# Kernel optimization log

Measured on AMD Instinct MI355X. Metric: run time of the kernel, lower is better.

The kernel has to match this reference:

```python
import jax, jax.numpy as jnp
import numpy as np

LAYER_START = 4
WIN = 2          # context_window_size (over the LAYER axis)
NORM_EPS = 1e-12 # F.normalize eps
COS_EPS = 1e-8   # cosine_similarity eps


def _alpha_for_k(sf, k, nlay):
    """Alignment/novelty weights for layer k. sf: [B, Ttok, Lay, H].
    Mirrors torch: left = tf[k-w:k] (empty when k<w due to python slicing),
    right = tf[k+1:k+w+1], self row last; QR of window_matrix.T."""
    left = list(range(k - WIN, k)) if k >= WIN else []
    right = list(range(k + 1, min(k + WIN + 1, nlay)))
    rows = left + right + [k]
    m = len(rows)  # 3..5
    W = sf[:, :, jnp.array(rows), :]          # [B,T,m,H]
    A = jnp.swapaxes(W, -1, -2)               # [B,T,H,m]  (window_matrix.T)
    _, R = jnp.linalg.qr(A)                   # reduced: R [B,T,m,m]
    r = R[..., :, -1]                         # [B,T,m]
    Rsub = R[..., :-1, :-1]                   # [B,T,m-1,m-1]
    coln = Rsub / jnp.maximum(jnp.linalg.norm(Rsub, axis=-2, keepdims=True), NORM_EPS)
    row_mean = jnp.mean(coln, axis=-1)        # mean over columns -> [B,T,m-1]
    align = jnp.sum(row_mean * R[..., :-1, -1], axis=-1) / jnp.linalg.norm(r[..., :-1], axis=-1)
    align = 1.0 / (align * m * 2)
    novelty = jnp.abs(r[..., -1]) / jnp.linalg.norm(r, axis=-1)
    return align, novelty


def wk_forward(all_hidden_states, attention_mask):
    # [NL,B,T,H] -> [B, Lay, T, H] after layer_start slice
    emb = jnp.transpose(all_hidden_states, (1, 0, 2, 3))[:, LAYER_START:, :, :]
    B, Lay, T, H = emb.shape
    ntok = T - 1  # attention_mask is all-ones: unmask_num = sum(mask) - 1
    sf = jnp.transpose(emb[:, :, :ntok, :], (0, 2, 1, 3))  # [B,Ttok,Lay,H]
    aligns, novs = [], []
    for k in range(Lay):  # small fixed loop over 9 layers
        a, n = _alpha_for_k(sf, k, Lay)
        aligns.append(a)
        novs.append(n)
    align = jnp.stack(aligns, axis=-1)  # [B,Ttok,Lay]
    nov = jnp.stack(novs, axis=-1)
    align = align / jnp.sum(align, axis=-1, keepdims=True)
    nov = nov / jnp.sum(nov, axis=-1, keepdims=True)
    alpha = align + nov
    alpha = alpha / jnp.sum(alpha, axis=-1, keepdims=True)
    token_emb = jnp.einsum('btl,btlh->bth', alpha, sf)  # unify_token output per token
    # unify_sentence: per-token variance (unbiased) of consecutive-layer cosine sims
    a, b = sf[:, :, 1:, :], sf[:, :, :-1, :]
    num = jnp.sum(a * b, axis=-1)
    den = jnp.maximum(jnp.linalg.norm(a, axis=-1) * jnp.linalg.norm(b, axis=-1), COS_EPS)
    sims = num / den                              # [B,Ttok,Lay-1]
    var_tok = jnp.var(sims, axis=-1, ddof=1)      # torch.var default unbiased
    var_tok = var_tok / jnp.sum(var_tok, axis=-1, keepdims=True)
    return jnp.einsum('bt,bth->bh', var_tok, token_emb)  # [B,H]


def setup_inputs() -> dict:
    key = jax.random.key(0)
    NL, B, T, H = 13, 8, 512, 768
    all_hidden_states = jax.random.normal(key, (NL, B, T, H), dtype=jnp.float32)
    attention_mask = jnp.ones((B, T), dtype=jnp.int32)
    return {"all_hidden_states": all_hidden_states, "attention_mask": attention_mask}


def reference(all_hidden_states, attention_mask):
    return wk_forward(all_hidden_states, attention_mask)
```

## Files before the change

### kernel.cpp

```cpp
#include <hip/hip_runtime.h>
#include <math.h>

#define B_DIM 8
#define T_DIM 512
#define H_DIM 768
#define NTOK 511
#define NLAY 9
#define LAYER_START 4
#define NBAND 35
#define TCHUNK 128

__device__ float g_part[B_DIM * TCHUNK * H_DIM];
__device__ float g_varp[B_DIM * TCHUNK];

#define BOFF(d) ((d)*9 - (d) * ((d)-1) / 2)

template <int CTRL>
__device__ __forceinline__ float dpp_mov(float x) {
  return __builtin_bit_cast(
      float, __builtin_amdgcn_update_dpp(0, __builtin_bit_cast(int, x), CTRL,
                                         0xF, 0xF, true));
}

__device__ __forceinline__ float wave_sum_dpp(float x) {
  x += dpp_mov<0x111>(x);
  x += dpp_mov<0x112>(x);
  x += dpp_mov<0x114>(x);
  x += dpp_mov<0x118>(x);
  x += dpp_mov<0x142>(x);
  x += dpp_mov<0x143>(x);
  return x;
}

__global__ __launch_bounds__(256, 2) void wk_a(const float* __restrict__ ahs) {
  const int chunk = blockIdx.x;
  const int b = blockIdx.y;
  const int wave = threadIdx.x >> 6;
  const int lane = threadIdx.x & 63;
  const int t_raw = chunk * 4 + wave;
  const bool active = (t_raw < NTOK);
  const int t = active ? t_raw : (NTOK - 1);

  __shared__ float sG[4][36];
  __shared__ float lds_out[4][H_DIM];
  __shared__ float lds_var[4];

  const size_t LSTR = (size_t)B_DIM * T_DIM * H_DIM;
  const float* lay0 =
      ahs + (size_t)LAYER_START * LSTR + ((size_t)b * T_DIM + t) * H_DIM;

  float4 v[NLAY][3];
#pragma unroll
  for (int l = 0; l < NLAY; ++l) {
    const float* base = lay0 + (size_t)l * LSTR;
#pragma unroll
    for (int s = 0; s < 3; ++s) {
      v[l][s] = *reinterpret_cast<const float4*>(base + s * 256 + lane * 4);
    }
  }

  float g[NBAND];
#pragma unroll
  for (int d = 0; d <= 4; ++d) {
#pragma unroll
    for (int i = 0; i + d < NLAY; ++i) {
      float s0 = 0.f;
#pragma unroll
      for (int s = 0; s < 3; ++s) {
        const float4 x = v[i][s], y = v[i + d][s];
        s0 += x.x * y.x + x.y * y.y + x.z * y.z + x.w * y.w;
      }
      g[BOFF(d) + i] = s0;
    }
  }

#pragma unroll
  for (int p = 0; p < NBAND; ++p) g[p] = wave_sum_dpp(g[p]);

  if (lane == 63) {
#pragma unroll
    for (int p = 0; p < NBAND; ++p) sG[wave][p] = g[p];
  }
  __syncthreads();

  const int k = lane < NLAY ? lane : NLAY - 1;
  const int nl = (k >= 2) ? 2 : 0;
  const int nrr = (NLAY - 1 - k) < 2 ? (NLAY - 1 - k) : 2;
  const int m = nl + nrr + 1;

  auto rowf = [&](int i) -> int {
    return (i < nl) ? (k - 2 + i) : ((i < nl + nrr) ? (k + 1 + i - nl) : k);
  };
  auto GK = [&](int i, int j) -> float {
    int a = rowf(i), c = rowf(j);
    int lo = a < c ? a : c;
    int d = (a < c ? c : a) - lo;
    return sG[wave][d * 9 - d * (d - 1) / 2 + lo];
  };

  float R[5][5];
#pragma unroll
  for (int j = 0; j < 5; ++j)
#pragma unroll
    for (int i = 0; i < 5; ++i) R[i][j] = 0.f;

#pragma unroll
  for (int j = 0; j < 5; ++j) {
    if (j < m) {
#pragma unroll
      for (int i = 0; i < 5; ++i) {
        if (i < j) {
          float s = GK(i, j);
#pragma unroll
          for (int p = 0; p < 4; ++p)
            if (p < i) s -= R[p][i] * R[p][j];
          R[i][j] = s / R[i][i];
        }
      }
      float sjj = GK(j, j);
#pragma unroll
      for (int p = 0; p < 4; ++p)
        if (p < j) sjj -= R[p][j] * R[p][j];
      R[j][j] = sqrtf(fmaxf(sjj, 0.f));
    }
  }

  float r[5];
#pragma unroll
  for (int i = 0; i < 5; ++i)
    r[i] = (m == 3) ? R[i][2] : ((m == 4) ? R[i][3] : R[i][4]);

  float rowmean[4] = {0.f, 0.f, 0.f, 0.f};
#pragma unroll
  for (int j = 0; j < 4; ++j) {
    if (j < m - 1) {
      float cn = 0.f;
#pragma unroll
      for (int i = 0; i < 4; ++i)
        if (i <= j) cn += R[i][j] * R[i][j];
      cn = fmaxf(sqrtf(cn), 1e-12f);
      float inv = 1.f / cn;
#pragma unroll
      for (int i = 0; i < 4; ++i)
        if (i < m - 1) rowmean[i] += R[i][j] * inv;
    }
  }

  const float inv_m1 = 1.f / (float)(m - 1);
  float dotv = 0.f, nrm2 = 0.f;
#pragma unroll
  for (int i = 0; i < 4; ++i) {
    if (i < m - 1) {
      dotv += (rowmean[i] * inv_m1) * r[i];
      nrm2 += r[i] * r[i];
    }
  }
  float align_raw = dotv / sqrtf(nrm2);
  float align_v = 1.f / (align_raw * (float)m * 2.f);
  float rlast = (m == 3) ? r[2] : ((m == 4) ? r[3] : r[4]);
  float nov_v = fabsf(rlast) / sqrtf(nrm2 + rlast * rlast);

  float al[NLAY], nv[NLAY];
  float asum = 0.f, nsum = 0.f;
#pragma unroll
  for (int l = 0; l < NLAY; ++l) {
    al[l] = __shfl(align_v, l, 64);
    nv[l] = __shfl(nov_v, l, 64);
    asum += al[l];
    nsum += nv[l];
  }
  float alpha[NLAY];
  float csum = 0.f;
#pragma unroll
  for (int l = 0; l < NLAY; ++l) {
    alpha[l] = al[l] / asum + nv[l] / nsum;
    csum += alpha[l];
  }
  const float inv_csum = 1.f / csum;

  float sims[NLAY - 1];
  float smean = 0.f;
#pragma unroll
  for (int j = 0; j < NLAY - 1; ++j) {
    float num = sG[wave][BOFF(1) + j];
    float den = fmaxf(sqrtf(sG[wave][j]) * sqrtf(sG[wave][j + 1]), 1e-8f);
    sims[j] = num / den;
    smean += sims[j];
  }
  smean *= (1.f / 8.f);
  float var = 0.f;
#pragma unroll
  for (int j = 0; j < NLAY - 1; ++j) {
    float d = sims[j] - smean;
    var += d * d;
  }
  var *= (1.f / 7.f);
  if (!active) var = 0.f;

  if (lane == 0) lds_var[wave] = var;

  float c[NLAY];
#pragma unroll
  for (int l = 0; l < NLAY; ++l) c[l] = var * alpha[l] * inv_csum;

#pragma unroll
  for (int s = 0; s < 3; ++s) {
    float4 o;
    o.x = 0.f; o.y = 0.f; o.z = 0.f; o.w = 0.f;
#pragma unroll
    for (int l = 0; l < NLAY; ++l) {
      o.x += c[l] * v[l][s].x;
      o.y += c[l] * v[l][s].y;
      o.z += c[l] * v[l][s].z;
      o.w += c[l] * v[l][s].w;
    }
    *reinterpret_cast<float4*>(&lds_out[wave][s * 256 + lane * 4]) = o;
  }
  __syncthreads();

  float* dst = g_part + ((size_t)(b * TCHUNK + chunk)) * H_DIM;
#pragma unroll
  for (int s = 0; s < 3; ++s) {
    int h = s * 256 + threadIdx.x;
    float sum = lds_out[0][h] + lds_out[1][h] + lds_out[2][h] + lds_out[3][h];
    dst[h] = sum;
  }
  if (threadIdx.x == 0) {
    g_varp[b * TCHUNK + chunk] =
        lds_var[0] + lds_var[1] + lds_var[2] + lds_var[3];
  }
}

__global__ __launch_bounds__(256) void wk_r(float* __restrict__ out) {
  const int b = blockIdx.y;
  const int h = blockIdx.x * 256 + threadIdx.x;

  float acc = 0.f;
#pragma unroll 8
  for (int j = 0; j < TCHUNK; ++j)
    acc += g_part[((size_t)(b * TCHUNK + j)) * H_DIM + h];

  float ssum = 0.f;
#pragma unroll 8
  for (int j = 0; j < TCHUNK; ++j) ssum += g_varp[b * TCHUNK + j];

  out[b * H_DIM + h] = acc / ssum;
}

extern "C" void kernel_launch(void* const* d_in, const int* in_sizes, int n_in,
                              void* d_out, int out_size, void* d_ws, size_t ws_size,
                              hipStream_t stream) {
  const float* ahs = (const float*)d_in[0];
  float* out = (float*)d_out;
  (void)d_ws; (void)ws_size;

  wk_a<<<dim3(TCHUNK, B_DIM), dim3(256), 0, stream>>>(ahs);
  wk_r<<<dim3(3, B_DIM), dim3(256), 0, stream>>>(out);
}
```

Before: 227.2 us.

## Split fused kernel into gram, per-token tail, weighted-sum and finalize kernels

The single fused kernel, which held all 9 layers in registers, is split into four kernels. A gram kernel streams the layers in 3 slices with lower register pressure. A per-token tail kernel runs the Cholesky/alpha math with one thread per token. A weighted-sum kernel then re-reads the hidden states to accumulate the alpha-weighted sums, followed by a final reduction. This is meant to raise occupancy and remove the lane-serialized QR math from the bandwidth-bound pass, but it reads the input tensor twice and adds launches and global round-trips.

Result: slower. 258.5 us (+13.8%).

```diff
diff --git a/kernel.cpp b/kernel.cpp
--- a/kernel.cpp
+++ b/kernel.cpp
@@ -8,12 +8,14 @@
 #define NLAY 9
 #define LAYER_START 4
 #define NBAND 35
-#define TCHUNK 128
-
-__device__ float g_part[B_DIM * TCHUNK * H_DIM];
-__device__ float g_varp[B_DIM * TCHUNK];
+#define NCHUNK 64
 
 #define BOFF(d) ((d)*9 - (d) * ((d)-1) / 2)
+
+__device__ float g_gram[B_DIM * T_DIM * NBAND];
+__device__ float g_w[B_DIM * NTOK * NLAY];
+__device__ float g_var[B_DIM * NTOK];
+__device__ float g_part[B_DIM * NCHUNK * H_DIM];
 
 template <int CTRL>
 __device__ __forceinline__ float dpp_mov(float x) {
@@ -21,7 +23,6 @@
       float, __builtin_amdgcn_update_dpp(0, __builtin_bit_cast(int, x), CTRL,
                                          0xF, 0xF, true));
 }
-
 __device__ __forceinline__ float wave_sum_dpp(float x) {
   x += dpp_mov<0x111>(x);
   x += dpp_mov<0x112>(x);
@@ -32,45 +33,38 @@
   return x;
 }
 
-__global__ __launch_bounds__(256, 2) void wk_a(const float* __restrict__ ahs) {
+__global__ __launch_bounds__(256, 4) void gram_k(const float* __restrict__ ahs) {
   const int chunk = blockIdx.x;
   const int b = blockIdx.y;
   const int wave = threadIdx.x >> 6;
   const int lane = threadIdx.x & 63;
   const int t_raw = chunk * 4 + wave;
-  const bool active = (t_raw < NTOK);
-  const int t = active ? t_raw : (NTOK - 1);
-
-  __shared__ float sG[4][36];
-  __shared__ float lds_out[4][H_DIM];
-  __shared__ float lds_var[4];
+  const int t = (t_raw < NTOK) ? t_raw : (NTOK - 1);
+
+  __shared__ float sGall[4][NBAND];
 
   const size_t LSTR = (size_t)B_DIM * T_DIM * H_DIM;
   const float* lay0 =
       ahs + (size_t)LAYER_START * LSTR + ((size_t)b * T_DIM + t) * H_DIM;
 
-  float4 v[NLAY][3];
-#pragma unroll
-  for (int l = 0; l < NLAY; ++l) {
-    const float* base = lay0 + (size_t)l * LSTR;
-#pragma unroll
-    for (int s = 0; s < 3; ++s) {
-      v[l][s] = *reinterpret_cast<const float4*>(base + s * 256 + lane * 4);
-    }
-  }
-
   float g[NBAND];
 #pragma unroll
-  for (int d = 0; d <= 4; ++d) {
-#pragma unroll
-    for (int i = 0; i + d < NLAY; ++i) {
-      float s0 = 0.f;
-#pragma unroll
-      for (int s = 0; s < 3; ++s) {
-        const float4 x = v[i][s], y = v[i + d][s];
-        s0 += x.x * y.x + x.y * y.y + x.z * y.z + x.w * y.w;
+  for (int p = 0; p < NBAND; ++p) g[p] = 0.f;
+
+#pragma unroll 1
+  for (int s = 0; s < 3; ++s) {
+    const float* p0 = lay0 + s * 256 + lane * 4;
+    float4 vs[NLAY];
+#pragma unroll
+    for (int l = 0; l < NLAY; ++l)
+      vs[l] = *reinterpret_cast<const float4*>(p0 + (size_t)l * LSTR);
+#pragma unroll
+    for (int d = 0; d <= 4; ++d) {
+#pragma unroll
+      for (int i = 0; i + d < NLAY; ++i) {
+        const float4 x = vs[i], y = vs[i + d];
+        g[BOFF(d) + i] += x.x * y.x + x.y * y.y + x.z * y.z + x.w * y.w;
       }
-      g[BOFF(d) + i] = s0;
     }
   }
 
@@ -79,23 +73,36 @@
 
   if (lane == 63) {
 #pragma unroll
-    for (int p = 0; p < NBAND; ++p) sG[wave][p] = g[p];
+    for (int p = 0; p < NBAND; ++p) sGall[wave][p] = g[p];
   }
   __syncthreads();
 
-  const int k = lane < NLAY ? lane : NLAY - 1;
-  const int nl = (k >= 2) ? 2 : 0;
-  const int nrr = (NLAY - 1 - k) < 2 ? (NLAY - 1 - k) : 2;
-  const int m = nl + nrr + 1;
-
-  auto rowf = [&](int i) -> int {
-    return (i < nl) ? (k - 2 + i) : ((i < nl + nrr) ? (k + 1 + i - nl) : k);
+  const int i = threadIdx.x;
+  if (i < 4 * NBAND) {
+    const int w = i / NBAND;
+    const int p = i - w * NBAND;
+    const int tr = chunk * 4 + w;
+    g_gram[((size_t)(b * T_DIM + tr)) * NBAND + p] = sGall[w][p];
+  }
+}
+
+template <int K>
+__device__ __forceinline__ void chol_one(const float* __restrict__ row,
+                                         float& A_out, float& N_out) {
+  constexpr int nl = (K >= 2) ? 2 : 0;
+  constexpr int nr = ((NLAY - 1 - K) < 2) ? (NLAY - 1 - K) : 2;
+  constexpr int m = nl + nr + 1;
+
+  struct Map {
+    static constexpr int rowf(int i) {
+      return (i < nl) ? (K - 2 + i) : ((i < nl + nr) ? (K + 1 + i - nl) : K);
+    }
   };
   auto GK = [&](int i, int j) -> float {
-    int a = rowf(i), c = rowf(j);
-    int lo = a < c ? a : c;
-    int d = (a < c ? c : a) - lo;
-    return sG[wave][d * 9 - d * (d - 1) / 2 + lo];
+    const int a = Map::rowf(i), c = Map::rowf(j);
+    const int lo = a < c ? a : c;
+    const int d = (a < c ? c : a) - lo;
+    return row[d * 9 - d * (d - 1) / 2 + lo];
   };
 
   float R[5][5];
@@ -127,8 +134,7 @@
 
   float r[5];
 #pragma unroll
-  for (int i = 0; i < 5; ++i)
-    r[i] = (m == 3) ? R[i][2] : ((m == 4) ? R[i][3] : R[i][4]);
+  for (int i = 0; i < 5; ++i) r[i] = R[i][m - 1];
 
   float rowmean[4] = {0.f, 0.f, 0.f, 0.f};
 #pragma unroll
@@ -139,14 +145,14 @@
       for (int i = 0; i < 4; ++i)
         if (i <= j) cn += R[i][j] * R[i][j];
       cn = fmaxf(sqrtf(cn), 1e-12f);
-      float inv = 1.f / cn;
+      const float inv = 1.f / cn;
 #pragma unroll
       for (int i = 0; i < 4; ++i)
         if (i < m - 1) rowmean[i] += R[i][j] * inv;
     }
   }
 
-  const float inv_m1 = 1.f / (float)(m - 1);
+  constexpr float inv_m1 = 1.f / (float)(m - 1);
   float dotv = 0.f, nrm2 = 0.f;
 #pragma unroll
   for (int i = 0; i < 4; ++i) {
@@ -155,20 +161,41 @@
       nrm2 += r[i] * r[i];
     }
   }
-  float align_raw = dotv / sqrtf(nrm2);
-  float align_v = 1.f / (align_raw * (float)m * 2.f);
-  float rlast = (m == 3) ? r[2] : ((m == 4) ? r[3] : r[4]);
-  float nov_v = fabsf(rlast) / sqrtf(nrm2 + rlast * rlast);
+  const float align_raw = dotv / sqrtf(nrm2);
+  A_out = 1.f / (align_raw * (float)m * 2.f);
+  const float rlast = r[m - 1];
+  N_out = fabsf(rlast) / sqrtf(nrm2 + rlast * rlast);
+}
+
+__global__ __launch_bounds__(64) void tail_k() {
+  const int tid = threadIdx.x;
+  const int tok = blockIdx.x * 64 + tid;
+  const bool valid = (tok < B_DIM * NTOK);
+  const int tk = valid ? tok : 0;
+  const int b = tk / NTOK;
+  const int t = tk - b * NTOK;
+
+  __shared__ float sB[64][NBAND + 2];
+
+  const float* gp = g_gram + ((size_t)(b * T_DIM + t)) * NBAND;
+#pragma unroll
+  for (int p = 0; p < NBAND; ++p) sB[tid][p] = gp[p];
+  const float* row = &sB[tid][0];
 
   float al[NLAY], nv[NLAY];
+  chol_one<0>(row, al[0], nv[0]);
+  chol_one<1>(row, al[1], nv[1]);
+  chol_one<2>(row, al[2], nv[2]);
+  chol_one<3>(row, al[3], nv[3]);
+  chol_one<4>(row, al[4], nv[4]);
+  chol_one<5>(row, al[5], nv[5]);
+  chol_one<6>(row, al[6], nv[6]);
+  chol_one<7>(row, al[7], nv[7]);
+  chol_one<8>(row, al[8], nv[8]);
+
   float asum = 0.f, nsum = 0.f;
 #pragma unroll
-  for (int l = 0; l < NLAY; ++l) {
-    al[l] = __shfl(align_v, l, 64);
-    nv[l] = __shfl(nov_v, l, 64);
-    asum += al[l];
-    nsum += nv[l];
-  }
+  for (int l = 0; l < NLAY; ++l) { asum += al[l]; nsum += nv[l]; }
   float alpha[NLAY];
   float csum = 0.f;
 #pragma unroll
@@ -182,8 +209,8 @@
   float smean = 0.f;
 #pragma unroll
   for (int j = 0; j < NLAY - 1; ++j) {
-    float num = sG[wave][BOFF(1) + j];
-    float den = fmaxf(sqrtf(sG[wave][j]) * sqrtf(sG[wave][j + 1]), 1e-8f);
+    const float num = row[BOFF(1) + j];
+    const float den = fmaxf(sqrtf(row[j]) * sqrtf(row[j + 1]), 1e-8f);
     sims[j] = num / den;
     smean += sims[j];
   }
@@ -191,60 +218,63 @@
   float var = 0.f;
 #pragma unroll
   for (int j = 0; j < NLAY - 1; ++j) {
-    float d = sims[j] - smean;
+    const float d = sims[j] - smean;
     var += d * d;
   }
   var *= (1.f / 7.f);
-  if (!active) var = 0.f;
-
-  if (lane == 0) lds_var[wave] = var;
-
-  float c[NLAY];
-#pragma unroll
-  for (int l = 0; l < NLAY; ++l) c[l] = var * alpha[l] * inv_csum;
-
-#pragma unroll
-  for (int s = 0; s < 3; ++s) {
-    float4 o;
-    o.x = 0.f; o.y = 0.f; o.z = 0.f; o.w = 0.f;
+
+  if (valid) {
+#pragma unroll
+    for (int l = 0; l < NLAY; ++l)
+      g_w[(size_t)tok * NLAY + l] = var * alpha[l] * inv_csum;
+    g_var[tok] = var;
+  }
+}
+
+__global__ __launch_bounds__(192) void wsum_k(const float* __restrict__ ahs) {
+  const int c = blockIdx.x;
+  const int b = blockIdx.y;
+  const int h4 = threadIdx.x;
+  const size_t LSTR = (size_t)B_DIM * T_DIM * H_DIM;
+
+  float4 acc;
+  acc.x = 0.f; acc.y = 0.f; acc.z = 0.f; acc.w = 0.f;
+
+#pragma unroll 1
+  for (int tt = 0; tt < 8; ++tt) {
+    const int t = c * 8 + tt;
+    if (t >= NTOK) break;
+    const float* wp = g_w + ((size_t)(b * NTOK + t)) * NLAY;
+    const float* vbase = ahs + (size_t)LAYER_START * LSTR +
+                         ((size_t)b * T_DIM + t) * H_DIM + h4 * 4;
 #pragma unroll
     for (int l = 0; l < NLAY; ++l) {
-      o.x += c[l] * v[l][s].x;
-      o.y += c[l] * v[l][s].y;
-      o.z += c[l] * v[l][s].z;
-      o.w += c[l] * v[l][s].w;
-    }
-    *reinterpret_cast<float4*>(&lds_out[wave][s * 256 + lane * 4]) = o;
-  }
-  __syncthreads();
-
-  float* dst = g_part + ((size_t)(b * TCHUNK + chunk)) * H_DIM;
-#pragma unroll
-  for (int s = 0; s < 3; ++s) {
-    int h = s * 256 + threadIdx.x;
-    float sum = lds_out[0][h] + lds_out[1][h] + lds_out[2][h] + lds_out[3][h];
-    dst[h] = sum;
-  }
-  if (threadIdx.x == 0) {
-    g_varp[b * TCHUNK + chunk] =
-        lds_var[0] + lds_var[1] + lds_var[2] + lds_var[3];
-  }
-}
-
-__global__ __launch_bounds__(256) void wk_r(float* __restrict__ out) {
+      const float wl = wp[l];
+      const float4 vv = *reinterpret_cast<const float4*>(vbase + (size_t)l * LSTR);
+      acc.x += wl * vv.x;
+      acc.y += wl * vv.y;
+      acc.z += wl * vv.z;
+      acc.w += wl * vv.w;
+    }
+  }
+  *reinterpret_cast<float4*>(g_part + ((size_t)(b * NCHUNK + c)) * H_DIM +
+                             h4 * 4) = acc;
+}
+
+__global__ __launch_bounds__(256) void fin_k(float* __restrict__ out) {
   const int b = blockIdx.y;
   const int h = blockIdx.x * 256 + threadIdx.x;
 
   float acc = 0.f;
 #pragma unroll 8
-  for (int j = 0; j < TCHUNK; ++j)
-    acc += g_part[((size_t)(b * TCHUNK + j)) * H_DIM + h];
-
-  float ssum = 0.f;
+  for (int cc = 0; cc < NCHUNK; ++cc)
+    acc += g_part[((size_t)(b * NCHUNK + cc)) * H_DIM + h];
+
+  float sv = 0.f;
 #pragma unroll 8
-  for (int j = 0; j < TCHUNK; ++j) ssum += g_varp[b * TCHUNK + j];
-
-  out[b * H_DIM + h] = acc / ssum;
+  for (int t = 0; t < NTOK; ++t) sv += g_var[b * NTOK + t];
+
+  out[b * H_DIM + h] = acc / sv;
 }
 
 extern "C" void kernel_launch(void* const* d_in, const int* in_sizes, int n_in,
@@ -254,6 +284,8 @@
   float* out = (float*)d_out;
   (void)d_ws; (void)ws_size;
 
-  wk_a<<<dim3(TCHUNK, B_DIM), dim3(256), 0, stream>>>(ahs);
-  wk_r<<<dim3(3, B_DIM), dim3(256), 0, stream>>>(out);
-}
+  gram_k<<<dim3(T_DIM / 4, B_DIM), dim3(256), 0, stream>>>(ahs);
+  tail_k<<<dim3((B_DIM * NTOK + 63) / 64), dim3(64), 0, stream>>>();
+  wsum_k<<<dim3(NCHUNK, B_DIM), dim3(192), 0, stream>>>(ahs);
+  fin_k<<<dim3(3, B_DIM), dim3(256), 0, stream>>>(out);
+}
```

## Split each token across three waves and write per-token partials

Applied to the files above, without the earlier changes.

Work is repartitioned so that one 192-thread block handles one token, with each of its three waves covering a 256-element slice of H. Gram dot products are combined across the waves through shared memory, and a single wave then runs the small QR/alpha math. This cuts per-thread register use (9 float4 loads instead of 27), raising occupancy and memory-level parallelism for the bandwidth-bound load. In exchange, every token writes a full H-length partial to global memory and the final reduction loops over 511 tokens instead of 128 chunks, which adds about 12MB of extra write and read traffic.

Result: slower. 269.8 us (+18.8%).

```diff
diff --git a/kernel.cpp b/kernel.cpp
--- a/kernel.cpp
+++ b/kernel.cpp
@@ -8,12 +8,11 @@
 #define NLAY 9
 #define LAYER_START 4
 #define NBAND 35
-#define TCHUNK 128
-
-__device__ float g_part[B_DIM * TCHUNK * H_DIM];
-__device__ float g_varp[B_DIM * TCHUNK];
 
 #define BOFF(d) ((d)*9 - (d) * ((d)-1) / 2)
+
+__device__ float g_part[B_DIM * NTOK * H_DIM];
+__device__ float g_var[B_DIM * NTOK];
 
 template <int CTRL>
 __device__ __forceinline__ float dpp_mov(float x) {
@@ -21,7 +20,6 @@
       float, __builtin_amdgcn_update_dpp(0, __builtin_bit_cast(int, x), CTRL,
                                          0xF, 0xF, true));
 }
-
 __device__ __forceinline__ float wave_sum_dpp(float x) {
   x += dpp_mov<0x111>(x);
   x += dpp_mov<0x112>(x);
@@ -32,219 +30,199 @@
   return x;
 }
 
-__global__ __launch_bounds__(256, 2) void wk_a(const float* __restrict__ ahs) {
-  const int chunk = blockIdx.x;
+__global__ __launch_bounds__(192, 4) void wk_main(const float* __restrict__ ahs) {
+  const int t = blockIdx.x;
   const int b = blockIdx.y;
-  const int wave = threadIdx.x >> 6;
+  const int w = threadIdx.x >> 6;
   const int lane = threadIdx.x & 63;
-  const int t_raw = chunk * 4 + wave;
-  const bool active = (t_raw < NTOK);
-  const int t = active ? t_raw : (NTOK - 1);
-
-  __shared__ float sG[4][36];
-  __shared__ float lds_out[4][H_DIM];
-  __shared__ float lds_var[4];
+
+  __shared__ float sG[3][NBAND];
+  __shared__ float sGc[NBAND + 1];
+  __shared__ float sC[NLAY + 1];
 
   const size_t LSTR = (size_t)B_DIM * T_DIM * H_DIM;
-  const float* lay0 =
-      ahs + (size_t)LAYER_START * LSTR + ((size_t)b * T_DIM + t) * H_DIM;
-
-  float4 v[NLAY][3];
+  const float* base = ahs + (size_t)LAYER_START * LSTR +
+                      ((size_t)b * T_DIM + t) * H_DIM + w * 256 + lane * 4;
+
+  float4 v[NLAY];
+#pragma unroll
+  for (int l = 0; l < NLAY; ++l)
+    v[l] = *reinterpret_cast<const float4*>(base + (size_t)l * LSTR);
+
+  float g[NBAND];
+#pragma unroll
+  for (int d = 0; d <= 4; ++d) {
+#pragma unroll
+    for (int i = 0; i + d < NLAY; ++i) {
+      const float4 x = v[i], y = v[i + d];
+      g[BOFF(d) + i] = x.x * y.x + x.y * y.y + x.z * y.z + x.w * y.w;
+    }
+  }
+
+#pragma unroll
+  for (int p = 0; p < NBAND; ++p) g[p] = wave_sum_dpp(g[p]);
+
+  if (lane == 63) {
+#pragma unroll
+    for (int p = 0; p < NBAND; ++p) sG[w][p] = g[p];
+  }
+  __syncthreads();
+
+  if (threadIdx.x < NBAND)
+    sGc[threadIdx.x] =
+        sG[0][threadIdx.x] + sG[1][threadIdx.x] + sG[2][threadIdx.x];
+  __syncthreads();
+
+  if (w == 0) {
+    const int k = lane < NLAY ? lane : NLAY - 1;
+    const int nl = (k >= 2) ? 2 : 0;
+    const int nrr = (NLAY - 1 - k) < 2 ? (NLAY - 1 - k) : 2;
+    const int m = nl + nrr + 1;
+
+    auto rowf = [&](int i) -> int {
+      return (i < nl) ? (k - 2 + i) : ((i < nl + nrr) ? (k + 1 + i - nl) : k);
+    };
+    auto GK = [&](int i, int j) -> float {
+      int a = rowf(i), c = rowf(j);
+      int lo = a < c ? a : c;
+      int d = (a < c ? c : a) - lo;
+      return sGc[d * 9 - d * (d - 1) / 2 + lo];
+    };
+
+    float R[5][5];
+#pragma unroll
+    for (int j = 0; j < 5; ++j)
+#pragma unroll
+      for (int i = 0; i < 5; ++i) R[i][j] = 0.f;
+
+#pragma unroll
+    for (int j = 0; j < 5; ++j) {
+      if (j < m) {
+#pragma unroll
+        for (int i = 0; i < 5; ++i) {
+          if (i < j) {
+            float s = GK(i, j);
+#pragma unroll
+            for (int p = 0; p < 4; ++p)
+              if (p < i) s -= R[p][i] * R[p][j];
+            R[i][j] = s / R[i][i];
+          }
+        }
+        float sjj = GK(j, j);
+#pragma unroll
+        for (int p = 0; p < 4; ++p)
+          if (p < j) sjj -= R[p][j] * R[p][j];
+        R[j][j] = sqrtf(fmaxf(sjj, 0.f));
+      }
+    }
+
+    float r[5];
+#pragma unroll
+    for (int i = 0; i < 5; ++i)
+      r[i] = (m == 3) ? R[i][2] : ((m == 4) ? R[i][3] : R[i][4]);
+
+    float rowmean[4] = {0.f, 0.f, 0.f, 0.f};
+#pragma unroll
+    for (int j = 0; j < 4; ++j) {
+      if (j < m - 1) {
+        float cn = 0.f;
+#pragma unroll
+        for (int i = 0; i < 4; ++i)
+          if (i <= j) cn += R[i][j] * R[i][j];
+        cn = fmaxf(sqrtf(cn), 1e-12f);
+        const float inv = 1.f / cn;
+#pragma unroll
+        for (int i = 0; i < 4; ++i)
+          if (i < m - 1) rowmean[i] += R[i][j] * inv;
+      }
+    }
+
+    const float inv_m1 = 1.f / (float)(m - 1);
+    float dotv = 0.f, nrm2 = 0.f;
+#pragma unroll
+    for (int i = 0; i < 4; ++i) {
+      if (i < m - 1) {
+        dotv += (rowmean[i] * inv_m1) * r[i];
+        nrm2 += r[i] * r[i];
+      }
+    }
+    const float align_raw = dotv / sqrtf(nrm2);
+    const float align_v = 1.f / (align_raw * (float)m * 2.f);
+    const float rlast = (m == 3) ? r[2] : ((m == 4) ? r[3] : r[4]);
+    const float nov_v = fabsf(rlast) / sqrtf(nrm2 + rlast * rlast);
+
+    float al[NLAY], nv[NLAY];
+    float asum = 0.f, nsum = 0.f;
+#pragma unroll
+    for (int l = 0; l < NLAY; ++l) {
+      al[l] = __shfl(align_v, l, 64);
+      nv[l] = __shfl(nov_v, l, 64);
+      asum += al[l];
+      nsum += nv[l];
+    }
+    float alpha[NLAY];
+    float csum = 0.f;
+#pragma unroll
+    for (int l = 0; l < NLAY; ++l) {
+      alpha[l] = al[l] / asum + nv[l] / nsum;
+      csum += alpha[l];
+    }
+    const float inv_csum = 1.f / csum;
+
+    float sims[NLAY - 1];
+    float smean = 0.f;
+#pragma unroll
+    for (int j = 0; j < NLAY - 1; ++j) {
+      const float num = sGc[BOFF(1) + j];
+      const float den = fmaxf(sqrtf(sGc[j]) * sqrtf(sGc[j + 1]), 1e-8f);
+      sims[j] = num / den;
+      smean += sims[j];
+    }
+    smean *= (1.f / 8.f);
+    float var = 0.f;
+#pragma unroll
+    for (int j = 0; j < NLAY - 1; ++j) {
+      const float d = sims[j] - smean;
+      var += d * d;
+    }
+    var *= (1.f / 7.f);
+
+    if (lane < NLAY) sC[lane] = var * alpha[lane] * inv_csum;
+    if (lane == 0) g_var[b * NTOK + t] = var;
+  }
+  __syncthreads();
+
+  float c[NLAY];
+#pragma unroll
+  for (int l = 0; l < NLAY; ++l) c[l] = sC[l];
+
+  float4 o;
+  o.x = 0.f; o.y = 0.f; o.z = 0.f; o.w = 0.f;
 #pragma unroll
   for (int l = 0; l < NLAY; ++l) {
-    const float* base = lay0 + (size_t)l * LSTR;
-#pragma unroll
-    for (int s = 0; s < 3; ++s) {
-      v[l][s] = *reinterpret_cast<const float4*>(base + s * 256 + lane * 4);
-    }
-  }
-
-  float g[NBAND];
-#pragma unroll
-  for (int d = 0; d <= 4; ++d) {
-#pragma unroll
-    for (int i = 0; i + d < NLAY; ++i) {
-      float s0 = 0.f;
-#pragma unroll
-      for (int s = 0; s < 3; ++s) {
-        const float4 x = v[i][s], y = v[i + d][s];
-        s0 += x.x * y.x + x.y * y.y + x.z * y.z + x.w * y.w;
-      }
-      g[BOFF(d) + i] = s0;
-    }
-  }
-
-#pragma unroll
-  for (int p = 0; p < NBAND; ++p) g[p] = wave_sum_dpp(g[p]);
-
-  if (lane == 63) {
-#pragma unroll
-    for (int p = 0; p < NBAND; ++p) sG[wave][p] = g[p];
-  }
-  __syncthreads();
-
-  const int k = lane < NLAY ? lane : NLAY - 1;
-  const int nl = (k >= 2) ? 2 : 0;
-  const int nrr = (NLAY - 1 - k) < 2 ? (NLAY - 1 - k) : 2;
-  const int m = nl + nrr + 1;
-
-  auto rowf = [&](int i) -> int {
-    return (i < nl) ? (k - 2 + i) : ((i < nl + nrr) ? (k + 1 + i - nl) : k);
-  };
-  auto GK = [&](int i, int j) -> float {
-    int a = rowf(i), c = rowf(j);
-    int lo = a < c ? a : c;
-    int d = (a < c ? c : a) - lo;
-    return sG[wave][d * 9 - d * (d - 1) / 2 + lo];
-  };
-
-  float R[5][5];
-#pragma unroll
-  for (int j = 0; j < 5; ++j)
-#pragma unroll
-    for (int i = 0; i < 5; ++i) R[i][j] = 0.f;
-
-#pragma unroll
-  for (int j = 0; j < 5; ++j) {
-    if (j < m) {
-#pragma unroll
-      for (int i = 0; i < 5; ++i) {
-        if (i < j) {
-          float s = GK(i, j);
-#pragma unroll
-          for (int p = 0; p < 4; ++p)
-            if (p < i) s -= R[p][i] * R[p][j];
-          R[i][j] = s / R[i][i];
-        }
-      }
-      float sjj = GK(j, j);
-#pragma unroll
-      for (int p = 0; p < 4; ++p)
-        if (p < j) sjj -= R[p][j] * R[p][j];
-      R[j][j] = sqrtf(fmaxf(sjj, 0.f));
-    }
-  }
-
-  float r[5];
-#pragma unroll
-  for (int i = 0; i < 5; ++i)
-    r[i] = (m == 3) ? R[i][2] : ((m == 4) ? R[i][3] : R[i][4]);
-
-  float rowmean[4] = {0.f, 0.f, 0.f, 0.f};
-#pragma unroll
-  for (int j = 0; j < 4; ++j) {
-    if (j < m - 1) {
-      float cn = 0.f;
-#pragma unroll
-      for (int i = 0; i < 4; ++i)
-        if (i <= j) cn += R[i][j] * R[i][j];
-      cn = fmaxf(sqrtf(cn), 1e-12f);
-      float inv = 1.f / cn;
-#pragma unroll
-      for (int i = 0; i < 4; ++i)
-        if (i < m - 1) rowmean[i] += R[i][j] * inv;
-    }
-  }
-
-  const float inv_m1 = 1.f / (float)(m - 1);
-  float dotv = 0.f, nrm2 = 0.f;
-#pragma unroll
-  for (int i = 0; i < 4; ++i) {
-    if (i < m - 1) {
-      dotv += (rowmean[i] * inv_m1) * r[i];
-      nrm2 += r[i] * r[i];
-    }
-  }
-  float align_raw = dotv / sqrtf(nrm2);
-  float align_v = 1.f / (align_raw * (float)m * 2.f);
-  float rlast = (m == 3) ? r[2] : ((m == 4) ? r[3] : r[4]);
-  float nov_v = fabsf(rlast) / sqrtf(nrm2 + rlast * rlast);
-
-  float al[NLAY], nv[NLAY];
-  float asum = 0.f, nsum = 0.f;
-#pragma unroll
-  for (int l = 0; l < NLAY; ++l) {
-    al[l] = __shfl(align_v, l, 64);
-    nv[l] = __shfl(nov_v, l, 64);
-    asum += al[l];
-    nsum += nv[l];
-  }
-  float alpha[NLAY];
-  float csum = 0.f;
-#pragma unroll
-  for (int l = 0; l < NLAY; ++l) {
-    alpha[l] = al[l] / asum + nv[l] / nsum;
-    csum += alpha[l];
-  }
-  const float inv_csum = 1.f / csum;
-
-  float sims[NLAY - 1];
-  float smean = 0.f;
-#pragma unroll
-  for (int j = 0; j < NLAY - 1; ++j) {
-    float num = sG[wave][BOFF(1) + j];
-    float den = fmaxf(sqrtf(sG[wave][j]) * sqrtf(sG[wave][j + 1]), 1e-8f);
-    sims[j] = num / den;
-    smean += sims[j];
-  }
-  smean *= (1.f / 8.f);
-  float var = 0.f;
-#pragma unroll
-  for (int j = 0; j < NLAY - 1; ++j) {
-    float d = sims[j] - smean;
-    var += d * d;
-  }
-  var *= (1.f / 7.f);
-  if (!active) var = 0.f;
-
-  if (lane == 0) lds_var[wave] = var;
-
-  float c[NLAY];
-#pragma unroll
-  for (int l = 0; l < NLAY; ++l) c[l] = var * alpha[l] * inv_csum;
-
-#pragma unroll
-  for (int s = 0; s < 3; ++s) {
-    float4 o;
-    o.x = 0.f; o.y = 0.f; o.z = 0.f; o.w = 0.f;
-#pragma unroll
-    for (int l = 0; l < NLAY; ++l) {
-      o.x += c[l] * v[l][s].x;
-      o.y += c[l] * v[l][s].y;
-      o.z += c[l] * v[l][s].z;
-      o.w += c[l] * v[l][s].w;
-    }
-    *reinterpret_cast<float4*>(&lds_out[wave][s * 256 + lane * 4]) = o;
-  }
-  __syncthreads();
-
-  float* dst = g_part + ((size_t)(b * TCHUNK + chunk)) * H_DIM;
-#pragma unroll
-  for (int s = 0; s < 3; ++s) {
-    int h = s * 256 + threadIdx.x;
-    float sum = lds_out[0][h] + lds_out[1][h] + lds_out[2][h] + lds_out[3][h];
-    dst[h] = sum;
-  }
-  if (threadIdx.x == 0) {
-    g_varp[b * TCHUNK + chunk] =
-        lds_var[0] + lds_var[1] + lds_var[2] + lds_var[3];
-  }
-}
-
-__global__ __launch_bounds__(256) void wk_r(float* __restrict__ out) {
+    o.x += c[l] * v[l].x;
+    o.y += c[l] * v[l].y;
+    o.z += c[l] * v[l].z;
+    o.w += c[l] * v[l].w;
+  }
+  *reinterpret_cast<float4*>(g_part + ((size_t)(b * NTOK + t)) * H_DIM +
+                             w * 256 + lane * 4) = o;
+}
+
+__global__ __launch_bounds__(256) void fin_k(float* __restrict__ out) {
   const int b = blockIdx.y;
   const int h = blockIdx.x * 256 + threadIdx.x;
 
   float acc = 0.f;
 #pragma unroll 8
-  for (int j = 0; j < TCHUNK; ++j)
-    acc += g_part[((size_t)(b * TCHUNK + j)) * H_DIM + h];
-
-  float ssum = 0.f;
+  for (int t = 0; t < NTOK; ++t)
+    acc += g_part[((size_t)(b * NTOK + t)) * H_DIM + h];
+
+  float sv = 0.f;
 #pragma unroll 8
-  for (int j = 0; j < TCHUNK; ++j) ssum += g_varp[b * TCHUNK + j];
-
-  out[b * H_DIM + h] = acc / ssum;
+  for (int t = 0; t < NTOK; ++t) sv += g_var[b * NTOK + t];
+
+  out[b * H_DIM + h] = acc / sv;
 }
 
 extern "C" void kernel_launch(void* const* d_in, const int* in_sizes, int n_in,
@@ -254,6 +232,6 @@
   float* out = (float*)d_out;
   (void)d_ws; (void)ws_size;
 
-  wk_a<<<dim3(TCHUNK, B_DIM), dim3(256), 0, stream>>>(ahs);
-  wk_r<<<dim3(3, B_DIM), dim3(256), 0, stream>>>(out);
-}
+  wk_main<<<dim3(NTOK, B_DIM), dim3(192), 0, stream>>>(ahs);
+  fin_k<<<dim3(3, B_DIM), dim3(256), 0, stream>>>(out);
+}
```
